# Performance work log

Hardware: AMD Instinct MI355X
Metric: run time of the kernel (lower is better)

Reference implementation:

```python
import jax, jax.numpy as jnp
import numpy as np

N, E, IN_DIM, HID, HEADS, LAYERS, NUM_STORES = 50000, 800000, 64, 128, 16, 3, 50
DH = HID // HEADS  # per-head dim = 8
EPS = 1e-5


def setup_inputs() -> dict:
    key = jax.random.key(0)
    ks = iter(jax.random.split(key, 40))
    def nrm(shape, scale):
        return jax.random.normal(next(ks), shape, dtype=jnp.float32) * scale
    inp = {}
    inp['x'] = jax.random.normal(next(ks), (N, IN_DIM), dtype=jnp.float32)
    inp['edge_index'] = jax.random.randint(next(ks), (2, E), 0, N, dtype=jnp.int32)
    inp['edge_weight'] = jax.random.uniform(next(ks), (E, 1), dtype=jnp.float32)
    inp['store_mask'] = jax.random.randint(next(ks), (N,), 0, NUM_STORES, dtype=jnp.int32)
    # input_proj: Linear + GELU + LayerNorm
    inp['in_W'] = nrm((IN_DIM, HID), IN_DIM ** -0.5)
    inp['in_b'] = jnp.zeros((HID,), jnp.float32)
    inp['in_g'] = jnp.ones((HID,), jnp.float32)
    inp['in_beta'] = jnp.zeros((HID,), jnp.float32)
    # 3 stacked GATv2 layers (stacked leading dim = layer)
    s = HID ** -0.5
    inp['gat_Wl'] = nrm((LAYERS, HID, HID), s)
    inp['gat_bl'] = jnp.zeros((LAYERS, HID), jnp.float32)
    inp['gat_Wr'] = nrm((LAYERS, HID, HID), s)
    inp['gat_br'] = jnp.zeros((LAYERS, HID), jnp.float32)
    inp['gat_We'] = nrm((LAYERS, 1, HID), 1.0)
    inp['gat_att'] = nrm((LAYERS, HEADS, DH), DH ** -0.5)
    inp['gat_bias'] = jnp.zeros((LAYERS, HID), jnp.float32)
    inp['blk_g'] = jnp.ones((LAYERS, HID), jnp.float32)
    inp['blk_b'] = jnp.zeros((LAYERS, HID), jnp.float32)
    # per-store context gate + final norm
    inp['ctx_W'] = nrm((HID, HID), s)
    inp['ctx_b'] = jnp.zeros((HID,), jnp.float32)
    inp['fin_g'] = jnp.ones((HID,), jnp.float32)
    inp['fin_b'] = jnp.zeros((HID,), jnp.float32)
    return inp


def layernorm(x, g, b):
    mu = jnp.mean(x, axis=-1, keepdims=True)
    v = jnp.mean((x - mu) ** 2, axis=-1, keepdims=True)
    return (x - mu) * jax.lax.rsqrt(v + EPS) * g + b


def gatv2_layer(x, src, dst, ea, Wl, bl, Wr, br, We, att, bias):
    # x: [N, HID]; src/dst: [Et]; ea: [Et, 1]
    n = x.shape[0]
    xl = (x @ Wl + bl).reshape(n, HEADS, DH)   # source transform
    xr = (x @ Wr + br).reshape(n, HEADS, DH)   # target transform
    ee = (ea @ We).reshape(-1, HEADS, DH)      # edge-attr embedding
    e = jax.nn.leaky_relu(xl[src] + xr[dst] + ee, 0.2)  # [Et, H, D]
    logit = jnp.einsum('ehd,hd->eh', e, att)             # [Et, H]
    # segment softmax over incoming edges of each target node
    mx = jax.ops.segment_max(logit, dst, num_segments=n)
    p = jnp.exp(logit - mx[dst])
    Z = jax.ops.segment_sum(p, dst, num_segments=n)
    alpha = p / (Z[dst] + 1e-16)
    msg = alpha[:, :, None] * xl[src]                    # [Et, H, D]
    agg = jax.ops.segment_sum(msg, dst, num_segments=n)  # [N, H, D]
    return agg.reshape(n, HEADS * DH) + bias


def forward(x, edge_index, edge_weight, store_mask, in_W, in_b, in_g, in_beta,
            gat_Wl, gat_bl, gat_Wr, gat_br, gat_We, gat_att, gat_bias,
            blk_g, blk_b, ctx_W, ctx_b, fin_g, fin_b):
    n = x.shape[0]
    h = layernorm(jax.nn.gelu(x @ in_W + in_b, approximate=False), in_g, in_beta)
    src, dst = edge_index[0], edge_index[1]
    # PyG add_self_loops with fill_value='mean': per-target mean of incoming edge attrs
    deg = jax.ops.segment_sum(jnp.ones(src.shape, h.dtype), dst, num_segments=n)
    loop_attr = jax.ops.segment_sum(edge_weight, dst, num_segments=n) / jnp.maximum(deg, 1.0)[:, None]
    loops = jnp.arange(n, dtype=src.dtype)
    srcf = jnp.concatenate([src, loops])
    dstf = jnp.concatenate([dst, loops])
    eaf = jnp.concatenate([edge_weight, loop_attr], axis=0)
    for l in range(LAYERS):  # residual block: post-norm residual around conv
        m = gatv2_layer(h, srcf, dstf, eaf, gat_Wl[l], gat_bl[l], gat_Wr[l], gat_br[l],
                        gat_We[l], gat_att[l], gat_bias[l])
        h = layernorm(h + m, blk_g[l], blk_b[l])
    # per-store segmented mean -> sigmoid gate -> scatter back
    cnt = jax.ops.segment_sum(jnp.ones((n,), h.dtype), store_mask, num_segments=NUM_STORES)
    means = jax.ops.segment_sum(h, store_mask, num_segments=NUM_STORES) / jnp.maximum(cnt, 1.0)[:, None]
    gate = jax.nn.sigmoid(means @ ctx_W + ctx_b)
    h = h + (gate * means)[store_mask]
    return layernorm(h, fin_g, fin_b)


def reference(x, edge_index, edge_weight, store_mask, in_W, in_b, in_g, in_beta,
              gat_Wl, gat_bl, gat_Wr, gat_br, gat_We, gat_att, gat_bias,
              blk_g, blk_b, ctx_W, ctx_b, fin_g, fin_b):
    return forward(x, edge_index, edge_weight, store_mask, in_W, in_b, in_g, in_beta,
                   gat_Wl, gat_bl, gat_Wr, gat_br, gat_We, gat_att, gat_bias,
                   blk_g, blk_b, ctx_W, ctx_b, fin_g, fin_b)
```

## Files before the change

kernel.cpp:

```cpp
#include <hip/hip_runtime.h>
#include <math.h>

#define NN 50000
#define EE 800000
#define ET (EE + NN)
#define HID 128
#define NSTORE 50
#define NBL 196
#define CNT_B 3125
#define XCV_B 3125
#define WCV_B 192
#define IWC_B 32
#define SCT_B 3321
#define GEMB 391
#define SSB 512

typedef unsigned short ushort_t;
typedef unsigned long long u64;
typedef __attribute__((ext_vector_type(8))) short bf8;
typedef __attribute__((ext_vector_type(4))) float f4;
typedef __attribute__((ext_vector_type(2))) float f2;
typedef __attribute__((ext_vector_type(4))) unsigned int u4;

__device__ __forceinline__ ushort_t f2b(float f) {
    union { float f; unsigned int i; } v; v.f = f;
    unsigned int r = (v.i + 0x7fffu + ((v.i >> 16) & 1u)) >> 16;
    return (ushort_t)r;
}
__device__ __forceinline__ f2 b2f2v(unsigned int u) {
    union { unsigned int i; float f; } lo, hi;
    lo.i = u << 16; hi.i = u & 0xffff0000u;
    f2 r; r.x = lo.f; r.y = hi.f; return r;
}
__device__ __forceinline__ unsigned int pk2(float lo, float hi) {
    return (unsigned int)f2b(lo) | ((unsigned int)f2b(hi) << 16);
}
__device__ __forceinline__ f2 max2(f2 a, f2 b) {
#if __has_builtin(__builtin_elementwise_max)
    return __builtin_elementwise_max(a, b);
#else
    f2 r; r.x = fmaxf(a.x, b.x); r.y = fmaxf(a.y, b.y); return r;
#endif
}

__global__ __launch_bounds__(256) void k_build(const int* __restrict__ ei, const float* __restrict__ ew,
                                               const float* __restrict__ x, const float* __restrict__ inW,
                                               const float* __restrict__ gWl, const float* __restrict__ gWr,
                                               ushort_t* __restrict__ xb, ushort_t* __restrict__ inWt,
                                               ushort_t* __restrict__ Wlt, ushort_t* __restrict__ Wrt,
                                               u64* __restrict__ packed, int* __restrict__ rank) {
    int b = blockIdx.x, t = threadIdx.x;
    if (b < CNT_B) {
        int i = b * 256 + t;
        int dst = ei[EE + i];
        unsigned int wfix = __float2uint_rn(ew[i] * 16777216.0f);
        u64 old = atomicAdd(&packed[dst], (1ULL << 44) | (u64)wfix);
        rank[i] = (int)(old >> 44);
        return;
    }
    if (b < CNT_B + XCV_B) {
        int i = ((b - CNT_B) * 256 + t) * 4;
        f4 v = *(const f4*)(x + i);
        uint2 p; p.x = pk2(v.x, v.y); p.y = pk2(v.z, v.w);
        *(uint2*)(xb + i) = p;
        return;
    }
    if (b < CNT_B + XCV_B + WCV_B) {
        int i = (b - CNT_B - XCV_B) * 256 + t;
        int l = i >> 14, r = i & 16383, nn2 = r >> 7, k = r & 127;
        Wlt[i] = f2b(gWl[(size_t)l * 16384 + k * 128 + nn2]);
        Wrt[i] = f2b(gWr[(size_t)l * 16384 + k * 128 + nn2]);
        return;
    }
    {
        int i = (b - CNT_B - XCV_B - WCV_B) * 256 + t;
        int c = i >> 6, k = i & 63;
        inWt[i] = f2b(inW[k * 128 + c]);
    }
}

__global__ __launch_bounds__(256) void k_inproj(const ushort_t* __restrict__ A,
                                                const ushort_t* __restrict__ Wt,
                                                const float* __restrict__ bias,
                                                const float* __restrict__ g,
                                                const float* __restrict__ be,
                                                ushort_t* __restrict__ hb) {
    const int K = 64;
    __shared__ float s1[2][128], s2[2][128];
    int lane = threadIdx.x & 63, w = threadIdx.x >> 6;
    int rw = w >> 1, cw = w & 1;
    int q = lane >> 4, l16 = lane & 15;
    int row0 = blockIdx.x * 128 + rw * 64;
    int col0 = cw * 64;
    bf8 z; for (int t = 0; t < 8; ++t) z[t] = 0;

    bf8 bfr[2][4];
#pragma unroll
    for (int kk = 0; kk < 2; ++kk)
#pragma unroll
        for (int j = 0; j < 4; ++j)
            bfr[kk][j] = *(const bf8*)(Wt + (size_t)(col0 + j * 16 + l16) * K + kk * 32 + q * 8);

    f4 acc[4][4];
#pragma unroll
    for (int i = 0; i < 4; ++i)
#pragma unroll
        for (int j = 0; j < 4; ++j) acc[i][j] = (f4)(0.f);

#pragma unroll
    for (int kk = 0; kk < 2; ++kk) {
        bf8 af[4];
#pragma unroll
        for (int i = 0; i < 4; ++i) {
            int r = row0 + i * 16 + l16;
            af[i] = (r < NN) ? *(const bf8*)(A + (size_t)r * K + kk * 32 + q * 8) : z;
        }
#pragma unroll
        for (int i = 0; i < 4; ++i)
#pragma unroll
            for (int j = 0; j < 4; ++j)
                acc[i][j] = __builtin_amdgcn_mfma_f32_16x16x32_bf16(af[i], bfr[kk][j], acc[i][j], 0, 0, 0);
    }
#pragma unroll
    for (int i = 0; i < 4; ++i) {
#pragma unroll
        for (int j = 0; j < 4; ++j) {
            float bv = bias[col0 + j * 16 + l16];
#pragma unroll
            for (int r = 0; r < 4; ++r) {
                float v = acc[i][j][r] + bv;
                v = 0.5f * v * (1.f + erff(v * 0.70710678118654752f));
                acc[i][j][r] = v;
            }
        }
    }
#pragma unroll
    for (int i = 0; i < 4; ++i) {
#pragma unroll
        for (int r = 0; r < 4; ++r) {
            float sm = acc[i][0][r] + acc[i][1][r] + acc[i][2][r] + acc[i][3][r];
            float sq = acc[i][0][r] * acc[i][0][r] + acc[i][1][r] * acc[i][1][r]
                     + acc[i][2][r] * acc[i][2][r] + acc[i][3][r] * acc[i][3][r];
#pragma unroll
            for (int k = 1; k < 16; k <<= 1) { sm += __shfl_xor(sm, k); sq += __shfl_xor(sq, k); }
            if (l16 == 0) {
                int rl = rw * 64 + i * 16 + q * 4 + r;
                s1[cw][rl] = sm; s2[cw][rl] = sq;
            }
        }
    }
    __syncthreads();
#pragma unroll
    for (int i = 0; i < 4; ++i) {
#pragma unroll
        for (int r = 0; r < 4; ++r) {
            int rl = rw * 64 + i * 16 + q * 4 + r;
            int gr = blockIdx.x * 128 + rl;
            if (gr >= NN) continue;
            float sm = s1[0][rl] + s1[1][rl];
            float sq = s2[0][rl] + s2[1][rl];
            float mu = sm * (1.f / 128.f);
            float var = sq * (1.f / 128.f) - mu * mu;
            float rinv = rsqrtf(var + 1e-5f);
#pragma unroll
            for (int j = 0; j < 4; ++j) {
                int gc = col0 + j * 16 + l16;
                float v = (acc[i][j][r] - mu) * rinv * g[gc] + be[gc];
                hb[(size_t)gr * HID + gc] = f2b(v);
            }
        }
    }
}

__global__ __launch_bounds__(256) void k_psum(const u64* __restrict__ packed, int* __restrict__ bsum) {
    int t = threadIdx.x, bidx = blockIdx.x;
    int i = bidx * 256 + t;
    int v = (i < NN) ? (int)(packed[i] >> 44) + 1 : 0;
#pragma unroll
    for (int d = 1; d < 64; d <<= 1) v += __shfl_xor(v, d);
    __shared__ int ws4[4];
    if ((t & 63) == 0) ws4[t >> 6] = v;
    __syncthreads();
    if (t == 0) bsum[bidx] = ws4[0] + ws4[1] + ws4[2] + ws4[3];
}

__global__ __launch_bounds__(256) void k_scanb(const int* __restrict__ bsum,
                                               int* __restrict__ bbase, int* __restrict__ offs) {
    __shared__ int s[256];
    int t = threadIdx.x;
    int v = (t < NBL) ? bsum[t] : 0;
    s[t] = v;
    __syncthreads();
    for (int d = 1; d < 256; d <<= 1) {
        int u = (t >= d) ? s[t - d] : 0;
        __syncthreads();
        s[t] += u;
        __syncthreads();
    }
    if (t < NBL) bbase[t] = s[t] - v;
    if (t == 0) offs[NN] = ET;
}

__global__ __launch_bounds__(256) void k_offs(const u64* __restrict__ packed,
                                              const int* __restrict__ bbase, int* __restrict__ offs) {
    __shared__ int wsum4[4];
    int t = threadIdx.x, bidx = blockIdx.x;
    int i = bidx * 256 + t;
    int v = (i < NN) ? (int)(packed[i] >> 44) + 1 : 0;
    int lane = t & 63, w = t >> 6;
    int sc = v;
#pragma unroll
    for (int d = 1; d < 64; d <<= 1) {
        int u = __shfl_up(sc, d);
        if (lane >= d) sc += u;
    }
    if (lane == 63) wsum4[w] = sc;
    __syncthreads();
    int wo = 0;
    for (int k = 0; k < w; ++k) wo += wsum4[k];
    if (i < NN) offs[i] = bbase[bidx] + wo + sc - v;
}

__global__ __launch_bounds__(256) void k_gemm2(const ushort_t* __restrict__ A,
                                               const ushort_t* __restrict__ Wt0,
                                               const ushort_t* __restrict__ Wt1,
                                               const float* __restrict__ b0,
                                               const float* __restrict__ b1,
                                               ushort_t* __restrict__ o0,
                                               ushort_t* __restrict__ o1, int n,
                                               const int* __restrict__ ei,
                                               const float* __restrict__ ew,
                                               const int* __restrict__ offs,
                                               const u64* __restrict__ packed,
                                               const int* __restrict__ rank,
                                               int2* __restrict__ csr) {
    int bid = blockIdx.x;
    if (bid >= 2 * GEMB) {
        int i = (bid - 2 * GEMB) * 256 + threadIdx.x;
        if (i < EE) {
            int src = ei[i], dst = ei[EE + i];
            int pos = offs[dst] + rank[i];
            int2 v; v.x = src; v.y = __float_as_int(ew[i]);
            csr[pos] = v;
        } else if (i < ET) {
            int nd = i - EE;
            u64 p = packed[nd];
            int deg = (int)(p >> 44);
            float wsf = (float)(p & ((1ULL << 44) - 1)) * (1.0f / 16777216.0f);
            float la = wsf / fmaxf((float)deg, 1.0f);
            int pos = offs[nd + 1] - 1;
            int2 v; v.x = nd; v.y = __float_as_int(la);
            csr[pos] = v;
        }
        return;
    }
    const int K = 128;
    int by = (bid >= GEMB) ? 1 : 0;
    int bx = by ? bid - GEMB : bid;
    const ushort_t* Wt = by ? Wt1 : Wt0;
    const float* bias = by ? b1 : b0;
    ushort_t* outb = by ? o1 : o0;
    int lane = threadIdx.x & 63, w = threadIdx.x >> 6;
    int rw = w >> 1, cw = w & 1;
    int q = lane >> 4, l16 = lane & 15;
    int row0 = bx * 128 + rw * 64;
    int col0 = cw * 64;
    bf8 z; for (int t = 0; t < 8; ++t) z[t] = 0;

    bf8 bfr[4][4];
#pragma unroll
    for (int kk = 0; kk < 4; ++kk)
#pragma unroll
        for (int j = 0; j < 4; ++j)
            bfr[kk][j] = *(const bf8*)(Wt + (size_t)(col0 + j * 16 + l16) * K + kk * 32 + q * 8);

    f4 acc[4][4];
#pragma unroll
    for (int i = 0; i < 4; ++i)
#pragma unroll
        for (int j = 0; j < 4; ++j) acc[i][j] = (f4)(0.f);

#pragma unroll
    for (int kk = 0; kk < 4; ++kk) {
        bf8 af[4];
#pragma unroll
        for (int i = 0; i < 4; ++i) {
            int r = row0 + i * 16 + l16;
            af[i] = (r < n) ? *(const bf8*)(A + (size_t)r * K + kk * 32 + q * 8) : z;
        }
#pragma unroll
        for (int i = 0; i < 4; ++i)
#pragma unroll
            for (int j = 0; j < 4; ++j)
                acc[i][j] = __builtin_amdgcn_mfma_f32_16x16x32_bf16(af[i], bfr[kk][j], acc[i][j], 0, 0, 0);
    }
#pragma unroll
    for (int i = 0; i < 4; ++i) {
        int gr0 = row0 + i * 16 + q * 4;
#pragma unroll
        for (int j = 0; j < 4; ++j) {
            int gc = col0 + j * 16 + l16;
            float bv = bias[gc];
#pragma unroll
            for (int r = 0; r < 4; ++r) {
                int gr = gr0 + r;
                if (gr < n) outb[(size_t)gr * HID + gc] = f2b(acc[i][j][r] + bv);
            }
        }
    }
}

__global__ __launch_bounds__(256) void k_attn(const ushort_t* __restrict__ xl,
                                              const ushort_t* __restrict__ xr,
                                              ushort_t* __restrict__ hb,
                                              const int* __restrict__ offs,
                                              const int2* __restrict__ csr,
                                              const float* __restrict__ We,
                                              const float* __restrict__ att,
                                              const float* __restrict__ gbias,
                                              const float* __restrict__ g,
                                              const float* __restrict__ b) {
    int wid = (blockIdx.x * 256 + threadIdx.x) >> 6;
    int lane = threadIdx.x & 63;
    if (wid >= NN) return;
    int hd = lane & 15;
    int grp = lane >> 4;
    int dbase = hd * 8;
    size_t base = (size_t)wid * HID;

    f2 xr2[4], at2[4], we2[4];
    {
        u4 uxr = *(const u4*)(xr + base + dbase);
        xr2[0] = b2f2v(uxr.x); xr2[1] = b2f2v(uxr.y);
        xr2[2] = b2f2v(uxr.z); xr2[3] = b2f2v(uxr.w);
        f4 a0 = *(const f4*)(att + dbase), a1 = *(const f4*)(att + dbase + 4);
        at2[0].x = a0.x; at2[0].y = a0.y; at2[1].x = a0.z; at2[1].y = a0.w;
        at2[2].x = a1.x; at2[2].y = a1.y; at2[3].x = a1.z; at2[3].y = a1.w;
        f4 w0 = *(const f4*)(We + dbase), w1 = *(const f4*)(We + dbase + 4);
        we2[0].x = w0.x; we2[0].y = w0.y; we2[1].x = w0.z; we2[1].y = w0.w;
        we2[2].x = w1.x; we2[2].y = w1.y; we2[3].x = w1.z; we2[3].y = w1.w;
    }
    int p0 = offs[wid], p1 = offs[wid + 1];
    float Z = 0.f;
    f2 acc2[4];
#pragma unroll
    for (int q = 0; q < 4; ++q) { acc2[q].x = 0.f; acc2[q].y = 0.f; }

#define QUAD(EJ, MASKED)                                                        \
    {                                                                           \
        int ei_ = (EJ) + grp;                                                   \
        int s_ = __shfl(sv, ei_);                                               \
        float ea_ = __shfl(evl, ei_);                                           \
        bool val_ = MASKED ? (ei_ < mm) : true;                                 \
        u4 ux_ = *(const u4*)(xl + (size_t)s_ * HID + dbase);                   \
        f2 x2_[4];                                                              \
        x2_[0] = b2f2v(ux_.x); x2_[1] = b2f2v(ux_.y);                           \
        x2_[2] = b2f2v(ux_.z); x2_[3] = b2f2v(ux_.w);                           \
        f2 lg2_; lg2_.x = 0.f; lg2_.y = 0.f;                                    \
        _Pragma("unroll")                                                       \
        for (int q_ = 0; q_ < 4; ++q_) {                                        \
            f2 t_ = (x2_[q_] + xr2[q_]) + ea_ * we2[q_];                        \
            t_ = max2(t_, t_ * 0.2f);                                           \
            lg2_ += at2[q_] * t_;                                               \
        }                                                                       \
        float w_ = val_ ? __expf(lg2_.x + lg2_.y) : 0.f;                        \
        Z += w_;                                                                \
        _Pragma("unroll")                                                       \
        for (int q_ = 0; q_ < 4; ++q_) acc2[q_] += w_ * x2_[q_];                \
    }

    for (int cb = p0; cb < p1; cb += 64) {
        int mm = min(64, p1 - cb);
        int2 m2 = (lane < mm) ? csr[cb + lane] : make_int2(0, 0);
        int sv = m2.x;
        float evl = __int_as_float(m2.y);
        int j = 0;
        for (; j + 8 <= mm; j += 8) { QUAD(j, false) QUAD(j + 4, false) }
        for (; j < mm; j += 4) QUAD(j, true)
    }
#undef QUAD

    Z += __shfl_xor(Z, 16); Z += __shfl_xor(Z, 32);
#pragma unroll
    for (int q = 0; q < 4; ++q) {
        acc2[q].x += __shfl_xor(acc2[q].x, 16);
        acc2[q].x += __shfl_xor(acc2[q].x, 32);
        acc2[q].y += __shfl_xor(acc2[q].y, 16);
        acc2[q].y += __shfl_xor(acc2[q].y, 32);
    }
    float inv = 1.f / (Z + 1e-16f);
    float acc[8] = {acc2[0].x, acc2[0].y, acc2[1].x, acc2[1].y,
                    acc2[2].x, acc2[2].y, acc2[3].x, acc2[3].y};

    u4 uh = *(const u4*)(hb + base + dbase);
    f2 hr0 = b2f2v(uh.x), hr1 = b2f2v(uh.y), hr2 = b2f2v(uh.z), hr3 = b2f2v(uh.w);
    float hres[8] = {hr0.x, hr0.y, hr1.x, hr1.y, hr2.x, hr2.y, hr3.x, hr3.y};
    f4 gb0 = *(const f4*)(gbias + dbase), gb1 = *(const f4*)(gbias + dbase + 4);
    float gb8[8] = {gb0.x, gb0.y, gb0.z, gb0.w, gb1.x, gb1.y, gb1.z, gb1.w};
    float o[8], sm = 0.f, sq = 0.f;
#pragma unroll
    for (int q = 0; q < 8; ++q) {
        o[q] = acc[q] * inv + gb8[q] + hres[q];
        sm += o[q]; sq += o[q] * o[q];
    }
#pragma unroll
    for (int k = 1; k < 16; k <<= 1) { sm += __shfl_xor(sm, k); sq += __shfl_xor(sq, k); }
    float mu = sm * (1.f / 128.f);
    float var = sq * (1.f / 128.f) - mu * mu;
    float rinv = rsqrtf(var + 1e-5f);
    f4 g0 = *(const f4*)(g + dbase), g1 = *(const f4*)(g + dbase + 4);
    float g8[8] = {g0.x, g0.y, g0.z, g0.w, g1.x, g1.y, g1.z, g1.w};
    f4 b0 = *(const f4*)(b + dbase), b1 = *(const f4*)(b + dbase + 4);
    float b8[8] = {b0.x, b0.y, b0.z, b0.w, b1.x, b1.y, b1.z, b1.w};
    float v8[8];
#pragma unroll
    for (int q = 0; q < 8; ++q) v8[q] = (o[q] - mu) * rinv * g8[q] + b8[q];
    if (grp == 0) {
        u4 hu;
        hu.x = pk2(v8[0], v8[1]); hu.y = pk2(v8[2], v8[3]);
        hu.z = pk2(v8[4], v8[5]); hu.w = pk2(v8[6], v8[7]);
        *(u4*)(hb + base + dbase) = hu;
    }
}

__global__ __launch_bounds__(256) void k_store_sum(const ushort_t* __restrict__ hb,
                                                   const int* __restrict__ mask,
                                                   float* __restrict__ psums,
                                                   int* __restrict__ pcnts) {
    __shared__ float ls[NSTORE * HID];
    __shared__ int lc[NSTORE];
    int t = threadIdx.x, bidx = blockIdx.x;
    for (int i = t; i < NSTORE * HID; i += 256) ls[i] = 0.f;
    if (t < NSTORE) lc[t] = 0;
    __syncthreads();
    int wid = bidx * 4 + (t >> 6);
    int lane = t & 63;
    int nw = SSB * 4;
    int d0 = lane * 2;
    for (int node = wid; node < NN; node += nw) {
        int s = mask[node];
        unsigned int hv = ((const unsigned int*)(hb + (size_t)node * HID))[lane];
        f2 v = b2f2v(hv);
        atomicAdd(&ls[s * HID + d0], v.x);
        atomicAdd(&ls[s * HID + d0 + 1], v.y);
        if (lane == 0) atomicAdd(&lc[s], 1);
    }
    __syncthreads();
    for (int i = t; i < NSTORE * HID; i += 256) psums[(size_t)bidx * (NSTORE * HID) + i] = ls[i];
    if (t < NSTORE) pcnts[bidx * NSTORE + t] = lc[t];
}

__global__ __launch_bounds__(256) void k_gate(const float* __restrict__ psums,
                                              const int* __restrict__ pcnts,
                                              const float* __restrict__ ctxW,
                                              const float* __restrict__ ctxb,
                                              float* __restrict__ gm) {
    __shared__ float h1[HID];
    __shared__ float mloc[HID];
    __shared__ int cw4[4];
    int s = blockIdx.x, t = threadIdx.x;
    int d = t & 127, half = t >> 7;
    float s0 = 0.f, s1 = 0.f, s2 = 0.f, s3 = 0.f;
    for (int b = half * 4; b < SSB; b += 8) {
        s0 += psums[(size_t)(b + 0) * (NSTORE * HID) + s * HID + d];
        s1 += psums[(size_t)(b + 1) * (NSTORE * HID) + s * HID + d];
        s2 += psums[(size_t)(b + 2) * (NSTORE * HID) + s * HID + d];
        s3 += psums[(size_t)(b + 3) * (NSTORE * HID) + s * HID + d];
    }
    float sum = (s0 + s1) + (s2 + s3);
    int c = pcnts[t * NSTORE + s] + pcnts[(t + 256) * NSTORE + s];
#pragma unroll
    for (int k = 1; k < 64; k <<= 1) c += __shfl_xor(c, k);
    if ((t & 63) == 0) cw4[t >> 6] = c;
    if (half) h1[d] = sum;
    __syncthreads();
    if (half == 0) {
        float tot = sum + h1[d];
        float cnt = fmaxf((float)(cw4[0] + cw4[1] + cw4[2] + cw4[3]), 1.f);
        mloc[d] = tot / cnt;
    }
    __syncthreads();
    if (half == 0) {
        float acc = ctxb[d];
        for (int j = 0; j < HID; ++j) acc += mloc[j] * ctxW[j * HID + d];
        float gate = 1.f / (1.f + __expf(-acc));
        gm[s * HID + d] = gate * mloc[d];
    }
}

__global__ __launch_bounds__(256) void k_final(const ushort_t* __restrict__ hb,
                                               const int* __restrict__ mask,
                                               const float* __restrict__ gm,
                                               const float* __restrict__ g,
                                               const float* __restrict__ b,
                                               float* __restrict__ out) {
    int wid = (blockIdx.x * 256 + threadIdx.x) >> 6;
    int lane = threadIdx.x & 63;
    if (wid >= NN) return;
    size_t base = (size_t)wid * HID;
    int s = mask[wid];
    int d0 = lane * 2, d1 = d0 + 1;
    unsigned int hv = ((const unsigned int*)(hb + base))[lane];
    f2 hvv = b2f2v(hv);
    float v0 = hvv.x + gm[s * HID + d0];
    float v1 = hvv.y + gm[s * HID + d1];
    float sm = v0 + v1, sq = v0 * v0 + v1 * v1;
#pragma unroll
    for (int k = 1; k < 64; k <<= 1) { sm += __shfl_xor(sm, k); sq += __shfl_xor(sq, k); }
    float mu = sm * (1.f / 128.f);
    float var = sq * (1.f / 128.f) - mu * mu;
    float r = rsqrtf(var + 1e-5f);
    out[base + d0] = (v0 - mu) * r * g[d0] + b[d0];
    out[base + d1] = (v1 - mu) * r * g[d1] + b[d1];
}

extern "C" void kernel_launch(void* const* d_in, const int* in_sizes, int n_in,
                              void* d_out, int out_size, void* d_ws, size_t ws_size,
                              hipStream_t stream) {
    const float* x      = (const float*)d_in[0];
    const int*   ei     = (const int*)d_in[1];
    const float* ew     = (const float*)d_in[2];
    const int*   smask  = (const int*)d_in[3];
    const float* inW    = (const float*)d_in[4];
    const float* inb    = (const float*)d_in[5];
    const float* ing    = (const float*)d_in[6];
    const float* inbeta = (const float*)d_in[7];
    const float* gWl    = (const float*)d_in[8];
    const float* gbl    = (const float*)d_in[9];
    const float* gWr    = (const float*)d_in[10];
    const float* gbr    = (const float*)d_in[11];
    const float* gWe    = (const float*)d_in[12];
    const float* gatt   = (const float*)d_in[13];
    const float* gbias  = (const float*)d_in[14];
    const float* blkg   = (const float*)d_in[15];
    const float* blkb   = (const float*)d_in[16];
    const float* ctxW   = (const float*)d_in[17];
    const float* ctxb   = (const float*)d_in[18];
    const float* fing   = (const float*)d_in[19];
    const float* finb   = (const float*)d_in[20];
    float* out = (float*)d_out;

    float* ws = (float*)d_ws;
    size_t o = 0;
    int2*     csr    = (int2*)(ws + o);     o += (size_t)ET * 2;
    float*    gm     = ws + o;              o += NSTORE * HID;
    int*      offs   = (int*)(ws + o);      o += 50004;
    int*      rank   = (int*)(ws + o);      o += EE;
    ushort_t* xb     = (ushort_t*)(ws + o); o += (size_t)NN * 64 / 2;
    ushort_t* hb     = (ushort_t*)(ws + o); o += (size_t)NN * HID / 2;
    ushort_t* xlb    = (ushort_t*)(ws + o); o += (size_t)NN * HID / 2;
    ushort_t* xrb    = (ushort_t*)(ws + o); o += (size_t)NN * HID / 2;
    ushort_t* inWt   = (ushort_t*)(ws + o); o += 128 * 64 / 2;
    ushort_t* Wlt    = (ushort_t*)(ws + o); o += 3 * 128 * 128 / 2;
    ushort_t* Wrt    = (ushort_t*)(ws + o); o += 3 * 128 * 128 / 2;
    int*      bsum   = (int*)(ws + o);      o += 256;
    int*      bbase  = (int*)(ws + o);      o += 256;
    float*    psums  = ws + o;              o += (size_t)SSB * NSTORE * HID;
    int*      pcnts  = (int*)(ws + o);      o += SSB * NSTORE;
    if (o & 1) ++o;
    float*    zbase  = ws + o;
    u64*      packed = (u64*)(ws + o);      o += (size_t)NN * 2;
    size_t zbytes = (size_t)(NN * 2) * 4;

    hipMemsetAsync((void*)zbase, 0, zbytes, stream);

    const int WB = NN / 4;

    k_build<<<CNT_B + XCV_B + WCV_B + IWC_B, 256, 0, stream>>>(ei, ew, x, inW, gWl, gWr,
                                                               xb, inWt, Wlt, Wrt, packed, rank);
    k_inproj<<<GEMB, 256, 0, stream>>>(xb, inWt, inb, ing, inbeta, hb);
    k_psum<<<NBL, 256, 0, stream>>>(packed, bsum);
    k_scanb<<<1, 256, 0, stream>>>(bsum, bbase, offs);
    k_offs<<<NBL, 256, 0, stream>>>(packed, bbase, offs);

    for (int l = 0; l < 3; ++l) {
        int nb = 2 * GEMB + (l == 0 ? SCT_B : 0);
        k_gemm2<<<nb, 256, 0, stream>>>(hb, Wlt + (size_t)l * HID * HID, Wrt + (size_t)l * HID * HID,
                                        gbl + l * HID, gbr + l * HID, xlb, xrb, NN,
                                        ei, ew, offs, packed, rank, csr);
        k_attn<<<WB, 256, 0, stream>>>(xlb, xrb, hb, offs, csr,
                                       gWe + l * HID, gatt + l * HID, gbias + l * HID,
                                       blkg + l * HID, blkb + l * HID);
    }

    k_store_sum<<<SSB, 256, 0, stream>>>(hb, smask, psums, pcnts);
    k_gate<<<NSTORE, 256, 0, stream>>>(psums, pcnts, ctxW, ctxb, gm);
    k_final<<<WB, 256, 0, stream>>>(hb, smask, gm, fing, finb, out);
}
```

Before: 504.6 us.

## Software-pipeline GAT neighbor gathers and store pre-scaled byte offsets in CSR

```diff
diff --git a/kernel.cpp b/kernel.cpp
--- a/kernel.cpp
+++ b/kernel.cpp
@@ -240,7 +240,7 @@
         if (i < EE) {
             int src = ei[i], dst = ei[EE + i];
             int pos = offs[dst] + rank[i];
-            int2 v; v.x = src; v.y = __float_as_int(ew[i]);
+            int2 v; v.x = src << 8; v.y = __float_as_int(ew[i]);
             csr[pos] = v;
         } else if (i < ET) {
             int nd = i - EE;
@@ -249,7 +249,7 @@
             float wsf = (float)(p & ((1ULL << 44) - 1)) * (1.0f / 16777216.0f);
             float la = wsf / fmaxf((float)deg, 1.0f);
             int pos = offs[nd + 1] - 1;
-            int2 v; v.x = nd; v.y = __float_as_int(la);
+            int2 v; v.x = nd << 8; v.y = __float_as_int(la);
             csr[pos] = v;
         }
         return;
@@ -326,6 +326,7 @@
     int hd = lane & 15;
     int grp = lane >> 4;
     int dbase = hd * 8;
+    int db2 = hd * 16;
     size_t base = (size_t)wid * HID;
 
     f2 xr2[4], at2[4], we2[4];
@@ -346,39 +347,52 @@
 #pragma unroll
     for (int q = 0; q < 4; ++q) { acc2[q].x = 0.f; acc2[q].y = 0.f; }
 
-#define QUAD(EJ, MASKED)                                                        \
-    {                                                                           \
-        int ei_ = (EJ) + grp;                                                   \
-        int s_ = __shfl(sv, ei_);                                               \
-        float ea_ = __shfl(evl, ei_);                                           \
-        bool val_ = MASKED ? (ei_ < mm) : true;                                 \
-        u4 ux_ = *(const u4*)(xl + (size_t)s_ * HID + dbase);                   \
-        f2 x2_[4];                                                              \
-        x2_[0] = b2f2v(ux_.x); x2_[1] = b2f2v(ux_.y);                           \
-        x2_[2] = b2f2v(ux_.z); x2_[3] = b2f2v(ux_.w);                           \
-        f2 lg2_; lg2_.x = 0.f; lg2_.y = 0.f;                                    \
-        _Pragma("unroll")                                                       \
-        for (int q_ = 0; q_ < 4; ++q_) {                                        \
-            f2 t_ = (x2_[q_] + xr2[q_]) + ea_ * we2[q_];                        \
-            t_ = max2(t_, t_ * 0.2f);                                           \
-            lg2_ += at2[q_] * t_;                                               \
-        }                                                                       \
-        float w_ = val_ ? __expf(lg2_.x + lg2_.y) : 0.f;                        \
-        Z += w_;                                                                \
-        _Pragma("unroll")                                                       \
-        for (int q_ = 0; q_ < 4; ++q_) acc2[q_] += w_ * x2_[q_];                \
-    }
-
-    for (int cb = p0; cb < p1; cb += 64) {
-        int mm = min(64, p1 - cb);
-        int2 m2 = (lane < mm) ? csr[cb + lane] : make_int2(0, 0);
-        int sv = m2.x;
-        float evl = __int_as_float(m2.y);
-        int j = 0;
-        for (; j + 8 <= mm; j += 8) { QUAD(j, false) QUAD(j + 4, false) }
-        for (; j < mm; j += 4) QUAD(j, true)
-    }
-#undef QUAD
+#define LOADQ(UX, EA, VM)                                                      \
+    {                                                                          \
+        int ei_ = e + grp;                                                     \
+        VM = (ei_ < p1);                                                       \
+        int2 m2_ = csr[VM ? ei_ : (p1 - 1)];                                   \
+        EA = __int_as_float(m2_.y);                                            \
+        UX = *(const u4*)((const char*)xl + (unsigned)m2_.x + db2);            \
+    }
+
+#define COMPQ(UX, EA, VM)                                                      \
+    {                                                                          \
+        f2 x2_[4];                                                             \
+        x2_[0] = b2f2v(UX.x); x2_[1] = b2f2v(UX.y);                            \
+        x2_[2] = b2f2v(UX.z); x2_[3] = b2f2v(UX.w);                            \
+        f2 lg2_; lg2_.x = 0.f; lg2_.y = 0.f;                                   \
+        _Pragma("unroll")                                                      \
+        for (int q_ = 0; q_ < 4; ++q_) {                                       \
+            f2 t_ = (x2_[q_] + xr2[q_]) + EA * we2[q_];                        \
+            t_ = max2(t_, t_ * 0.2f);                                          \
+            lg2_ += at2[q_] * t_;                                              \
+        }                                                                      \
+        float w_ = VM ? __expf(lg2_.x + lg2_.y) : 0.f;                         \
+        Z += w_;                                                               \
+        _Pragma("unroll")                                                      \
+        for (int q_ = 0; q_ < 4; ++q_) acc2[q_] += w_ * x2_[q_];               \
+    }
+
+    {
+        u4 uxA, uxB; float eaA, eaB; bool vA, vB;
+        int e = p0;
+        LOADQ(uxA, eaA, vA)
+        e += 4;
+        while (e < p1) {
+            LOADQ(uxB, eaB, vB)
+            e += 4;
+            COMPQ(uxA, eaA, vA)
+            if (e >= p1) { COMPQ(uxB, eaB, vB) goto redux; }
+            LOADQ(uxA, eaA, vA)
+            e += 4;
+            COMPQ(uxB, eaB, vB)
+        }
+        COMPQ(uxA, eaA, vA)
+    }
+redux:;
+#undef LOADQ
+#undef COMPQ
 
     Z += __shfl_xor(Z, 16); Z += __shfl_xor(Z, 32);
 #pragma unroll
```

Result: no change. 507.6 us (+0.6%).
